# Optimization experiments

Hardware: AMD Instinct MI355X
Metric: run time of the kernel (lower is better)

The kernel has to match this reference:

```python
import jax, jax.numpy as jnp
import numpy as np

FG_THRESH = 0.5  # fg_iou_thresh in RetinaNetLoss.__init__
BG_THRESH = 0.4  # bg_iou_thresh
BELOW_LOW_QUALITY = -1
BETWEEN_THRESHOLDS = -2


def _make_boxes(key, lead_shape, img_size=800.0, max_wh=128.0):
    # Build valid xyxy boxes (x1<x2, y1<y2) inside an img_size image.
    k1, k2 = jax.random.split(key)
    cxcy = jax.random.uniform(k1, lead_shape + (2,), minval=0.0, maxval=img_size)
    wh = jax.random.uniform(k2, lead_shape + (2,), minval=8.0, maxval=max_wh)
    return jnp.concatenate([cxcy - wh * 0.5, cxcy + wh * 0.5], axis=-1)


def setup_inputs() -> dict:
    key = jax.random.key(0)
    kb, ka = jax.random.split(key)
    B, G, A = 8, 64, 120000
    gt_boxes = _make_boxes(kb, (B, G))                 # [B, G, 4] per-image gt boxes
    anchors = _make_boxes(ka, (A,), max_wh=256.0)      # [A, 4] shared anchors
    return {"gt_boxes": gt_boxes, "anchors": anchors}


def _box_iou(boxes1, boxes2):
    # boxes1 [G,4], boxes2 [A,4] -> IoU [G,A] (torchvision box_ops.box_iou)
    area1 = (boxes1[:, 2] - boxes1[:, 0]) * (boxes1[:, 3] - boxes1[:, 1])  # [G]
    area2 = (boxes2[:, 2] - boxes2[:, 0]) * (boxes2[:, 3] - boxes2[:, 1])  # [A]
    lt = jnp.maximum(boxes1[:, None, :2], boxes2[None, :, :2])  # [G,A,2]
    rb = jnp.minimum(boxes1[:, None, 2:], boxes2[None, :, 2:])  # [G,A,2]
    wh = jnp.clip(rb - lt, 0.0)
    inter = wh[..., 0] * wh[..., 1]  # [G,A]
    return inter / (area1[:, None] + area2[None, :] - inter)


def _match(quality):
    # torchvision Matcher(0.5, 0.4, allow_low_quality_matches=True) on quality [G,A]
    matched_vals = quality.max(axis=0)                      # [A] best IoU per anchor
    all_matches = jnp.argmax(quality, axis=0)               # [A] pre-threshold matches
    matches = jnp.where(matched_vals < BG_THRESH, BELOW_LOW_QUALITY, all_matches)
    matches = jnp.where((matched_vals >= BG_THRESH) & (matched_vals < FG_THRESH),
                        BETWEEN_THRESHOLDS, matches)
    # low-quality match recovery: anchors achieving the per-gt max keep their match
    highest_per_gt = quality.max(axis=1, keepdims=True)     # [G,1]
    pred_update = (quality == highest_per_gt).any(axis=0)   # [A]
    matches = jnp.where(pred_update, all_matches, matches)
    return matches.astype(jnp.int64), matched_vals


def reference(gt_boxes, anchors):
    # gt_boxes [B,G,4], anchors [A,4] -> matched_idxs [B,A] int64, matched_vals [B,A]
    def per_image(boxes):
        return _match(_box_iou(boxes, anchors))
    matched_idxs, matched_vals = jax.vmap(per_image)(gt_boxes)
    return matched_idxs, matched_vals
```

## Files before the change

kernel.cpp:

```cpp
#include <hip/hip_runtime.h>


static constexpr int G = 64;
static constexpr int NCELL = 256;

__device__ __forceinline__ float opaque(float x) {
    asm volatile("" : "+v"(x));
    return x;
}

__device__ __forceinline__ int vindex(int i) {
    asm volatile("" : "+v"(i));
    return i;
}

__device__ __forceinline__ float box_area(float x1, float y1, float x2, float y2) {
    return opaque(__fmul_rn(__fsub_rn(x2, x1), __fsub_rn(y2, y1)));
}

__device__ __forceinline__ float inter_area(float gx1, float gy1, float gx2, float gy2,
                                            float ax1, float ay1, float ax2, float ay2) {
    float ltx = fmaxf(gx1, ax1);
    float lty = fmaxf(gy1, ay1);
    float rbx = fminf(gx2, ax2);
    float rby = fminf(gy2, ay2);
    float w = fmaxf(__fsub_rn(rbx, ltx), 0.0f);
    float h = fmaxf(__fsub_rn(rby, lty), 0.0f);
    return opaque(__fmul_rn(w, h));
}

__device__ __forceinline__ float div_rn(float n, float d) {
    float r = __builtin_amdgcn_rcpf(d);
    float e = fmaf(-d, r, 1.0f);
    r = fmaf(e, r, r);
    float q = __fmul_rn(n, r);
    float s = fmaf(-d, q, n);
    q = fmaf(s, r, q);
    s = fmaf(-d, q, n);
    q = fmaf(s, r, q);
    return q;
}

#define DPP_MAX_STAGE(x, ctrl)                                                   \
    do {                                                                         \
        int _yi = __builtin_amdgcn_update_dpp(__float_as_int(x),                 \
                                              __float_as_int(x), (ctrl),         \
                                              0xf, 0xf, false);                  \
        (x) = fmaxf((x), __int_as_float(_yi));                                   \
    } while (0)

#define DPP_MIN_STAGE(x, ctrl)                                                   \
    do {                                                                         \
        int _yi = __builtin_amdgcn_update_dpp(__float_as_int(x),                 \
                                              __float_as_int(x), (ctrl),         \
                                              0xf, 0xf, false);                  \
        (x) = fminf((x), __int_as_float(_yi));                                   \
    } while (0)

__device__ __forceinline__ float wave_max_lane63(float x) {
    DPP_MAX_STAGE(x, 0xB1);
    DPP_MAX_STAGE(x, 0x4E);
    DPP_MAX_STAGE(x, 0x141);
    DPP_MAX_STAGE(x, 0x140);
    DPP_MAX_STAGE(x, 0x142);
    DPP_MAX_STAGE(x, 0x143);
    return x;
}

__device__ __forceinline__ float wave_min_lane63(float x) {
    DPP_MIN_STAGE(x, 0xB1);
    DPP_MIN_STAGE(x, 0x4E);
    DPP_MIN_STAGE(x, 0x141);
    DPP_MIN_STAGE(x, 0x140);
    DPP_MIN_STAGE(x, 0x142);
    DPP_MIN_STAGE(x, 0x143);
    return x;
}

__device__ __forceinline__ float lane63_bcast(float x) {
    return __int_as_float(__builtin_amdgcn_readlane(__float_as_int(x), 63));
}

__global__ void k_init(const float* __restrict__ gt, unsigned int* __restrict__ hpg,
                       float* __restrict__ gab, int BG) {
    int i = blockIdx.x * 256 + threadIdx.x;
    if (i < BG) {
        hpg[i] = 0u;
        float4 gb = ((const float4*)gt)[i];
        gab[i] = box_area(gb.x, gb.y, gb.z, gb.w);
    }
}

__device__ __forceinline__ int cell_of(float4 ab) {
    float cx = (ab.x + ab.z) * 0.5f;
    float cy = (ab.y + ab.w) * 0.5f;
    int cxi = (int)(cx * 0.02f); cxi = cxi < 0 ? 0 : (cxi > 15 ? 15 : cxi);
    int cyi = (int)(cy * 0.02f); cyi = cyi < 0 ? 0 : (cyi > 15 ? 15 : cyi);
    return cyi * 16 + cxi;
}

__global__ void k_count(const float* __restrict__ anchors,
                        unsigned int* __restrict__ bh, int A, int NB) {
    __shared__ unsigned int h[NCELL];
    int t = threadIdx.x;
    h[t] = 0u;
    __syncthreads();
    int a = blockIdx.x * 256 + t;
    if (a < A) atomicAdd(&h[cell_of(((const float4*)anchors)[a])], 1u);
    __syncthreads();
    bh[(size_t)t * NB + blockIdx.x] = h[t];
}

__global__ void k_rowscan(unsigned int* __restrict__ bh,
                          unsigned int* __restrict__ cellTot, int NB) {
    const int c = blockIdx.x;
    unsigned int* row = bh + (size_t)c * NB;
    __shared__ unsigned int s[256];
    __shared__ unsigned int carry;
    if (threadIdx.x == 0) carry = 0u;
    __syncthreads();
    for (int base = 0; base < NB; base += 256) {
        int i = base + threadIdx.x;
        unsigned int v = (i < NB) ? row[i] : 0u;
        s[threadIdx.x] = v;
        __syncthreads();
        for (int d = 1; d < 256; d <<= 1) {
            unsigned int add = (threadIdx.x >= d) ? s[threadIdx.x - d] : 0u;
            __syncthreads();
            s[threadIdx.x] += add;
            __syncthreads();
        }
        unsigned int excl = s[threadIdx.x] - v + carry;
        if (i < NB) row[i] = excl;
        __syncthreads();
        if (threadIdx.x == 255) carry += s[255];
        __syncthreads();
    }
    if (threadIdx.x == 0) cellTot[c] = carry;
}

__global__ void k_base(const unsigned int* __restrict__ cellTot,
                       unsigned int* __restrict__ cellBase) {
    __shared__ unsigned int s[NCELL];
    int t = threadIdx.x;
    unsigned int v = cellTot[t];
    s[t] = v;
    __syncthreads();
    for (int d = 1; d < NCELL; d <<= 1) {
        unsigned int add = (t >= d) ? s[t - d] : 0u;
        __syncthreads();
        s[t] += add;
        __syncthreads();
    }
    cellBase[t] = s[t] - v;
}

__global__ void k_scat(const float* __restrict__ anchors,
                       const unsigned int* __restrict__ bh,
                       const unsigned int* __restrict__ cellBase,
                       float* __restrict__ sortedA,
                       int* __restrict__ orig, int A, int NB) {
    __shared__ unsigned int h[NCELL];
    int t = threadIdx.x;
    h[t] = 0u;
    __syncthreads();
    int a = blockIdx.x * 256 + t;
    if (a < A) {
        float4 ab = ((const float4*)anchors)[a];
        int c = cell_of(ab);
        unsigned int lr = atomicAdd(&h[c], 1u);
        unsigned int pos = cellBase[c] + bh[(size_t)c * NB + blockIdx.x] + lr;
        ((float4*)sortedA)[pos] = ab;
        orig[pos] = a;
    }
}

template <bool STORE>
__global__ __launch_bounds__(256, 4)
void pass1_k(const float* __restrict__ gt,
             const float* __restrict__ anchors,
             const float* __restrict__ gab,
             unsigned int* __restrict__ hpg,
             unsigned int* __restrict__ sredg,
             float* __restrict__ vmaxA,
             int* __restrict__ amaxA,
             int A, int nchunks) {
    const int b = blockIdx.y;
    const int t = threadIdx.x;

    __shared__ unsigned int sred[G];
    if (t < G) sred[t] = 0u;
    __syncthreads();

    const int base = blockIdx.x * 1024;
    float ax1[4], ay1[4], ax2[4], ay2[4], aar[4];
    bool val[4];
#pragma unroll
    for (int k = 0; k < 4; ++k) {
        int a = base + k * 256 + t;
        val[k] = (a < A);
        float4 ab = ((const float4*)anchors)[val[k] ? a : 0];
        ax1[k] = val[k] ? ab.x : 3.0e38f;
        ay1[k] = val[k] ? ab.y : 3.0e38f;
        ax2[k] = val[k] ? ab.z : -3.0e38f;
        ay2[k] = val[k] ? ab.w : -3.0e38f;
        aar[k] = val[k] ? box_area(ax1[k], ay1[k], ax2[k], ay2[k]) : 0.0f;
    }

    float wx1 = fminf(fminf(ax1[0], ax1[1]), fminf(ax1[2], ax1[3]));
    float wy1 = fminf(fminf(ay1[0], ay1[1]), fminf(ay1[2], ay1[3]));
    float wx2 = fmaxf(fmaxf(ax2[0], ax2[1]), fmaxf(ax2[2], ax2[3]));
    float wy2 = fmaxf(fmaxf(ay2[0], ay2[1]), fmaxf(ay2[2], ay2[3]));
    wx1 = lane63_bcast(wave_min_lane63(wx1));
    wy1 = lane63_bcast(wave_min_lane63(wy1));
    wx2 = lane63_bcast(wave_max_lane63(wx2));
    wy2 = lane63_bcast(wave_max_lane63(wy2));

    const float4* gtb = (const float4*)gt + (size_t)b * G;
    const float* gas = gab + b * G;

    float vmax[4] = {0.0f, 0.0f, 0.0f, 0.0f};
    int amax[4] = {0, 0, 0, 0};

#pragma unroll 4
    for (int g = 0; g < G; ++g) {
        const int gv = vindex(g);
        const float4 gb = gtb[gv];
        float tlx = fmaxf(gb.x, wx1), trx = fminf(gb.z, wx2);
        float tly = fmaxf(gb.y, wy1), tby = fminf(gb.w, wy2);
        if ((trx > tlx) && (tby > tly)) {
            float inter[4];
#pragma unroll
            for (int k = 0; k < 4; ++k)
                inter[k] = inter_area(gb.x, gb.y, gb.z, gb.w,
                                      ax1[k], ay1[k], ax2[k], ay2[k]);
            float itest = fmaxf(fmaxf(inter[0], inter[1]),
                                fmaxf(inter[2], inter[3]));
            if (__any(itest > 0.0f)) {
                const float ga = gas[gv];
                float m = 0.0f;
#pragma unroll
                for (int k = 0; k < 4; ++k) {
                    float denom = __fsub_rn(__fadd_rn(ga, aar[k]), inter[k]);
                    float q = div_rn(inter[k], denom);
                    if constexpr (STORE) {
                        if (q > vmax[k]) { vmax[k] = q; amax[k] = g; }
                    }
                    m = fmaxf(m, q);
                }
                m = wave_max_lane63(m);
                if ((t & 63) == 63)
                    atomicMax(&sred[g], __float_as_uint(m));
            }
        }
    }

    if constexpr (STORE) {
#pragma unroll
        for (int k = 0; k < 4; ++k) {
            if (!val[k]) continue;
            size_t idx = (size_t)b * A + (base + k * 256 + t);
            vmaxA[idx] = vmax[k];
            amaxA[idx] = amax[k];
        }
    }

    __syncthreads();
    if (t < G) {
        atomicMax(&hpg[b * G + t], sred[t]);
        if constexpr (STORE)
            sredg[(size_t)(b * nchunks + blockIdx.x) * G + t] = sred[t];
    }
}

template <bool SCATTER>
__global__ __launch_bounds__(256, 8)
void pass2_lite(const float* __restrict__ gt,
                const float* __restrict__ anchors,
                const float* __restrict__ gab,
                const unsigned int* __restrict__ hpg,
                const unsigned int* __restrict__ sredg,
                const float* __restrict__ vmaxA,
                const int* __restrict__ amaxA,
                const int* __restrict__ orig,
                float* __restrict__ out_idx,
                float* __restrict__ out_val,
                int A, int nchunks) {
    const int b = blockIdx.y;
    const int t = threadIdx.x;
    const int base = blockIdx.x * 1024;

    const unsigned int* sb = sredg + (size_t)(b * nchunks + blockIdx.x) * G;
    const unsigned int* hb = hpg + b * G;

    unsigned long long E = 0ull;
#pragma unroll 16
    for (int g = 0; g < G; ++g)
        E |= (sb[g] == hb[g]) ? (1ull << g) : 0ull;

    bool pu[4] = {false, false, false, false};

    if (E != 0ull) {
        const float4* gtb = (const float4*)gt + (size_t)b * G;
        const float* gas = gab + b * G;
        float ax1[4], ay1[4], ax2[4], ay2[4], aar[4];
#pragma unroll
        for (int k = 0; k < 4; ++k) {
            int a = base + k * 256 + t;
            bool v = (a < A);
            float4 ab = ((const float4*)anchors)[v ? a : 0];
            ax1[k] = v ? ab.x : 3.0e38f;
            ay1[k] = v ? ab.y : 3.0e38f;
            ax2[k] = v ? ab.z : -3.0e38f;
            ay2[k] = v ? ab.w : -3.0e38f;
            aar[k] = v ? box_area(ax1[k], ay1[k], ax2[k], ay2[k]) : 0.0f;
        }
        unsigned long long e = E;
        while (e) {
            int g = __builtin_ctzll(e);
            e &= e - 1;
            float4 gb = gtb[g];
            float ga = gas[g];
            float hgf = __uint_as_float(hb[g]);
#pragma unroll
            for (int k = 0; k < 4; ++k) {
                float inter = inter_area(gb.x, gb.y, gb.z, gb.w,
                                         ax1[k], ay1[k], ax2[k], ay2[k]);
                float denom = __fsub_rn(__fadd_rn(ga, aar[k]), inter);
                float q = div_rn(inter, denom);
                pu[k] = pu[k] | (q == hgf);
            }
        }
    }

#pragma unroll
    for (int k = 0; k < 4; ++k) {
        int a = base + k * 256 + t;
        if (a >= A) continue;
        size_t idx = (size_t)b * A + a;
        float vm = vmaxA[idx];
        int am = amaxA[idx];
        int m;
        if (pu[k]) {
            m = am;
        } else if (vm < 0.4f) {
            m = -1;
        } else if (vm < 0.5f) {
            m = -2;
        } else {
            m = am;
        }
        size_t o = SCATTER ? ((size_t)b * A + orig[a]) : idx;
        out_idx[o] = (float)m;
        out_val[o] = vm;
    }
}

extern "C" void kernel_launch(void* const* d_in, const int* in_sizes, int n_in,
                              void* d_out, int out_size, void* d_ws, size_t ws_size,
                              hipStream_t stream) {
    const float* gt = (const float*)d_in[0];
    const float* anchors = (const float*)d_in[1];
    const int BG = in_sizes[0] / 4;
    const int B = BG / G;
    const int A = in_sizes[1] / 4;

    const int nchunks = (A + 1023) / 1024;
    const int NB = (A + 255) / 256;

    unsigned int* ws = (unsigned int*)d_ws;
    unsigned int* hpg = ws;
    float* gab = (float*)(ws + 512);
    unsigned int* cellBase = ws + 1024;
    unsigned int* cellTot = ws + 1280;
    unsigned int* bh = ws + 1536;
    size_t soff = 1536 + (size_t)NB * 256;
    soff = (soff + 3) & ~(size_t)3;
    float* sortedA = (float*)(ws + soff);
    int* orig = (int*)(ws + soff + 4 * (size_t)A);
    unsigned int* sredg = ws + soff + 5 * (size_t)A;
    size_t voff = soff + 5 * (size_t)A + (size_t)nchunks * B * G;
    float* vmaxA = (float*)(ws + voff);
    int* amaxA = (int*)(vmaxA + (size_t)B * A);
    const size_t need = (voff + 2 * (size_t)B * A) * 4;
    const bool sorted = (ws_size >= need);

    float* out_idx = (float*)d_out;
    float* out_val = out_idx + (size_t)B * A;

    k_init<<<(BG + 255) / 256, 256, 0, stream>>>(gt, hpg, gab, BG);

    dim3 g1(nchunks, B);
    if (sorted) {
        k_count<<<NB, 256, 0, stream>>>(anchors, bh, A, NB);
        k_rowscan<<<NCELL, 256, 0, stream>>>(bh, cellTot, NB);
        k_base<<<1, NCELL, 0, stream>>>(cellTot, cellBase);
        k_scat<<<NB, 256, 0, stream>>>(anchors, bh, cellBase, sortedA, orig, A, NB);
        pass1_k<true><<<g1, 256, 0, stream>>>(gt, sortedA, gab, hpg, sredg,
                                              vmaxA, amaxA, A, nchunks);
        pass2_lite<true><<<g1, 256, 0, stream>>>(gt, sortedA, gab, hpg, sredg,
                                                 vmaxA, amaxA, orig,
                                                 out_idx, out_val, A, nchunks);
    } else {
        pass1_k<true><<<g1, 256, 0, stream>>>(gt, anchors, gab, hpg, sredg,
                                              vmaxA, amaxA, A, nchunks);
        pass2_lite<false><<<g1, 256, 0, stream>>>(gt, anchors, gab, hpg, sredg,
                                                  vmaxA, amaxA, orig,
                                                  out_idx, out_val, A, nchunks);
    }
}
```

Measured before the change: 80.40 us.

## Write final outputs in pass1, patch low-quality matches only, fuse init/base kernels

Pass1 now applies the threshold logic and writes matched indices and values straight to the output, and the second pass only rewrites indices for anchors that hit a per-gt maximum. Blocks with no such candidate exit early. This removes the vmax workspace round-trip and the full rewrite of both outputs in the second pass. The k_init work is folded into k_count and the k_base scan into k_scat, removing two launches. The cost is that every k_scat block redundantly rescans the 256 cell totals. In the fallback path k_count now also runs its full anchor histogram just to do the init work.

```diff
diff --git a/kernel.cpp b/kernel.cpp
--- a/kernel.cpp
+++ b/kernel.cpp
@@ -81,16 +81,6 @@
     return __int_as_float(__builtin_amdgcn_readlane(__float_as_int(x), 63));
 }
 
-__global__ void k_init(const float* __restrict__ gt, unsigned int* __restrict__ hpg,
-                       float* __restrict__ gab, int BG) {
-    int i = blockIdx.x * 256 + threadIdx.x;
-    if (i < BG) {
-        hpg[i] = 0u;
-        float4 gb = ((const float4*)gt)[i];
-        gab[i] = box_area(gb.x, gb.y, gb.z, gb.w);
-    }
-}
-
 __device__ __forceinline__ int cell_of(float4 ab) {
     float cx = (ab.x + ab.z) * 0.5f;
     float cy = (ab.y + ab.w) * 0.5f;
@@ -99,10 +89,20 @@
     return cyi * 16 + cxi;
 }
 
-__global__ void k_count(const float* __restrict__ anchors,
-                        unsigned int* __restrict__ bh, int A, int NB) {
+__global__ void k_count(const float* __restrict__ gt,
+                        const float* __restrict__ anchors,
+                        unsigned int* __restrict__ bh,
+                        unsigned int* __restrict__ hpg,
+                        float* __restrict__ gab,
+                        int A, int NB, int BG) {
+    int t = threadIdx.x;
+    int gi = blockIdx.x * 256 + t;
+    if (gi < BG) {
+        hpg[gi] = 0u;
+        float4 gb = ((const float4*)gt)[gi];
+        gab[gi] = box_area(gb.x, gb.y, gb.z, gb.w);
+    }
     __shared__ unsigned int h[NCELL];
-    int t = threadIdx.x;
     h[t] = 0u;
     __syncthreads();
     int a = blockIdx.x * 256 + t;
@@ -139,51 +139,49 @@
     if (threadIdx.x == 0) cellTot[c] = carry;
 }
 
-__global__ void k_base(const unsigned int* __restrict__ cellTot,
-                       unsigned int* __restrict__ cellBase) {
-    __shared__ unsigned int s[NCELL];
+__global__ void k_scat(const float* __restrict__ anchors,
+                       const unsigned int* __restrict__ bh,
+                       const unsigned int* __restrict__ cellTot,
+                       float* __restrict__ sortedA,
+                       int* __restrict__ orig, int A, int NB) {
+    __shared__ unsigned int cb[NCELL];
+    __shared__ unsigned int tot[NCELL];
+    __shared__ unsigned int h[NCELL];
     int t = threadIdx.x;
     unsigned int v = cellTot[t];
-    s[t] = v;
+    cb[t] = v;
+    tot[t] = v;
+    h[t] = 0u;
     __syncthreads();
     for (int d = 1; d < NCELL; d <<= 1) {
-        unsigned int add = (t >= d) ? s[t - d] : 0u;
-        __syncthreads();
-        s[t] += add;
-        __syncthreads();
-    }
-    cellBase[t] = s[t] - v;
-}
-
-__global__ void k_scat(const float* __restrict__ anchors,
-                       const unsigned int* __restrict__ bh,
-                       const unsigned int* __restrict__ cellBase,
-                       float* __restrict__ sortedA,
-                       int* __restrict__ orig, int A, int NB) {
-    __shared__ unsigned int h[NCELL];
-    int t = threadIdx.x;
-    h[t] = 0u;
-    __syncthreads();
+        unsigned int add = (t >= d) ? cb[t - d] : 0u;
+        __syncthreads();
+        cb[t] += add;
+        __syncthreads();
+    }
     int a = blockIdx.x * 256 + t;
     if (a < A) {
         float4 ab = ((const float4*)anchors)[a];
         int c = cell_of(ab);
         unsigned int lr = atomicAdd(&h[c], 1u);
-        unsigned int pos = cellBase[c] + bh[(size_t)c * NB + blockIdx.x] + lr;
+        unsigned int base = cb[c] - tot[c];
+        unsigned int pos = base + bh[(size_t)c * NB + blockIdx.x] + lr;
         ((float4*)sortedA)[pos] = ab;
         orig[pos] = a;
     }
 }
 
-template <bool STORE>
+template <bool SCATTER>
 __global__ __launch_bounds__(256, 4)
 void pass1_k(const float* __restrict__ gt,
              const float* __restrict__ anchors,
              const float* __restrict__ gab,
              unsigned int* __restrict__ hpg,
              unsigned int* __restrict__ sredg,
-             float* __restrict__ vmaxA,
              int* __restrict__ amaxA,
+             const int* __restrict__ orig,
+             float* __restrict__ out_idx,
+             float* __restrict__ out_val,
              int A, int nchunks) {
     const int b = blockIdx.y;
     const int t = threadIdx.x;
@@ -243,9 +241,7 @@
                 for (int k = 0; k < 4; ++k) {
                     float denom = __fsub_rn(__fadd_rn(ga, aar[k]), inter[k]);
                     float q = div_rn(inter[k], denom);
-                    if constexpr (STORE) {
-                        if (q > vmax[k]) { vmax[k] = q; amax[k] = g; }
-                    }
+                    if (q > vmax[k]) { vmax[k] = q; amax[k] = g; }
                     m = fmaxf(m, q);
                 }
                 m = wave_max_lane63(m);
@@ -255,37 +251,40 @@
         }
     }
 
-    if constexpr (STORE) {
-#pragma unroll
-        for (int k = 0; k < 4; ++k) {
-            if (!val[k]) continue;
-            size_t idx = (size_t)b * A + (base + k * 256 + t);
-            vmaxA[idx] = vmax[k];
-            amaxA[idx] = amax[k];
-        }
+#pragma unroll
+    for (int k = 0; k < 4; ++k) {
+        if (!val[k]) continue;
+        int a = base + k * 256 + t;
+        size_t sidx = (size_t)b * A + a;
+        amaxA[sidx] = amax[k];
+        int mt;
+        if (vmax[k] < 0.4f) mt = -1;
+        else if (vmax[k] < 0.5f) mt = -2;
+        else mt = amax[k];
+        int ao = SCATTER ? orig[a] : a;
+        size_t o = (size_t)b * A + ao;
+        out_idx[o] = (float)mt;
+        out_val[o] = vmax[k];
     }
 
     __syncthreads();
     if (t < G) {
         atomicMax(&hpg[b * G + t], sred[t]);
-        if constexpr (STORE)
-            sredg[(size_t)(b * nchunks + blockIdx.x) * G + t] = sred[t];
+        sredg[(size_t)(b * nchunks + blockIdx.x) * G + t] = sred[t];
     }
 }
 
 template <bool SCATTER>
 __global__ __launch_bounds__(256, 8)
-void pass2_lite(const float* __restrict__ gt,
-                const float* __restrict__ anchors,
-                const float* __restrict__ gab,
-                const unsigned int* __restrict__ hpg,
-                const unsigned int* __restrict__ sredg,
-                const float* __restrict__ vmaxA,
-                const int* __restrict__ amaxA,
-                const int* __restrict__ orig,
-                float* __restrict__ out_idx,
-                float* __restrict__ out_val,
-                int A, int nchunks) {
+void k_patch(const float* __restrict__ gt,
+             const float* __restrict__ anchors,
+             const float* __restrict__ gab,
+             const unsigned int* __restrict__ hpg,
+             const unsigned int* __restrict__ sredg,
+             const int* __restrict__ amaxA,
+             const int* __restrict__ orig,
+             float* __restrict__ out_idx,
+             int A, int nchunks) {
     const int b = blockIdx.y;
     const int t = threadIdx.x;
     const int base = blockIdx.x * 1024;
@@ -297,62 +296,48 @@
 #pragma unroll 16
     for (int g = 0; g < G; ++g)
         E |= (sb[g] == hb[g]) ? (1ull << g) : 0ull;
-
-    bool pu[4] = {false, false, false, false};
-
-    if (E != 0ull) {
-        const float4* gtb = (const float4*)gt + (size_t)b * G;
-        const float* gas = gab + b * G;
-        float ax1[4], ay1[4], ax2[4], ay2[4], aar[4];
-#pragma unroll
-        for (int k = 0; k < 4; ++k) {
-            int a = base + k * 256 + t;
-            bool v = (a < A);
-            float4 ab = ((const float4*)anchors)[v ? a : 0];
-            ax1[k] = v ? ab.x : 3.0e38f;
-            ay1[k] = v ? ab.y : 3.0e38f;
-            ax2[k] = v ? ab.z : -3.0e38f;
-            ay2[k] = v ? ab.w : -3.0e38f;
-            aar[k] = v ? box_area(ax1[k], ay1[k], ax2[k], ay2[k]) : 0.0f;
-        }
-        unsigned long long e = E;
-        while (e) {
-            int g = __builtin_ctzll(e);
-            e &= e - 1;
-            float4 gb = gtb[g];
-            float ga = gas[g];
-            float hgf = __uint_as_float(hb[g]);
-#pragma unroll
-            for (int k = 0; k < 4; ++k) {
-                float inter = inter_area(gb.x, gb.y, gb.z, gb.w,
-                                         ax1[k], ay1[k], ax2[k], ay2[k]);
-                float denom = __fsub_rn(__fadd_rn(ga, aar[k]), inter);
-                float q = div_rn(inter, denom);
-                pu[k] = pu[k] | (q == hgf);
-            }
-        }
-    }
-
+    if (E == 0ull) return;
+
+    const float4* gtb = (const float4*)gt + (size_t)b * G;
+    const float* gas = gab + b * G;
+    float ax1[4], ay1[4], ax2[4], ay2[4], aar[4];
+    bool val[4];
 #pragma unroll
     for (int k = 0; k < 4; ++k) {
         int a = base + k * 256 + t;
-        if (a >= A) continue;
-        size_t idx = (size_t)b * A + a;
-        float vm = vmaxA[idx];
-        int am = amaxA[idx];
-        int m;
-        if (pu[k]) {
-            m = am;
-        } else if (vm < 0.4f) {
-            m = -1;
-        } else if (vm < 0.5f) {
-            m = -2;
-        } else {
-            m = am;
+        val[k] = (a < A);
+        float4 ab = ((const float4*)anchors)[val[k] ? a : 0];
+        ax1[k] = val[k] ? ab.x : 3.0e38f;
+        ay1[k] = val[k] ? ab.y : 3.0e38f;
+        ax2[k] = val[k] ? ab.z : -3.0e38f;
+        ay2[k] = val[k] ? ab.w : -3.0e38f;
+        aar[k] = val[k] ? box_area(ax1[k], ay1[k], ax2[k], ay2[k]) : 0.0f;
+    }
+
+    bool pu[4] = {false, false, false, false};
+    unsigned long long e = E;
+    while (e) {
+        int g = __builtin_ctzll(e);
+        e &= e - 1;
+        float4 gb = gtb[g];
+        float ga = gas[g];
+        float hgf = __uint_as_float(hb[g]);
+#pragma unroll
+        for (int k = 0; k < 4; ++k) {
+            float inter = inter_area(gb.x, gb.y, gb.z, gb.w,
+                                     ax1[k], ay1[k], ax2[k], ay2[k]);
+            float denom = __fsub_rn(__fadd_rn(ga, aar[k]), inter);
+            float q = div_rn(inter, denom);
+            pu[k] = pu[k] | (q == hgf);
         }
-        size_t o = SCATTER ? ((size_t)b * A + orig[a]) : idx;
-        out_idx[o] = (float)m;
-        out_val[o] = vm;
+    }
+
+#pragma unroll
+    for (int k = 0; k < 4; ++k) {
+        int a = base + k * 256 + t;
+        if (!val[k] || !pu[k]) continue;
+        int ao = SCATTER ? orig[a] : a;
+        out_idx[(size_t)b * A + ao] = (float)amaxA[(size_t)b * A + a];
     }
 }
 
@@ -371,41 +356,37 @@
     unsigned int* ws = (unsigned int*)d_ws;
     unsigned int* hpg = ws;
     float* gab = (float*)(ws + 512);
-    unsigned int* cellBase = ws + 1024;
-    unsigned int* cellTot = ws + 1280;
-    unsigned int* bh = ws + 1536;
-    size_t soff = 1536 + (size_t)NB * 256;
+    unsigned int* cellTot = ws + 1024;
+    unsigned int* bh = ws + 1280;
+    size_t soff = 1280 + (size_t)NB * 256;
     soff = (soff + 3) & ~(size_t)3;
     float* sortedA = (float*)(ws + soff);
     int* orig = (int*)(ws + soff + 4 * (size_t)A);
     unsigned int* sredg = ws + soff + 5 * (size_t)A;
-    size_t voff = soff + 5 * (size_t)A + (size_t)nchunks * B * G;
-    float* vmaxA = (float*)(ws + voff);
-    int* amaxA = (int*)(vmaxA + (size_t)B * A);
-    const size_t need = (voff + 2 * (size_t)B * A) * 4;
+    size_t aoff = soff + 5 * (size_t)A + (size_t)nchunks * B * G;
+    int* amaxA = (int*)(ws + aoff);
+    const size_t need = (aoff + (size_t)B * A) * 4;
     const bool sorted = (ws_size >= need);
 
     float* out_idx = (float*)d_out;
     float* out_val = out_idx + (size_t)B * A;
 
-    k_init<<<(BG + 255) / 256, 256, 0, stream>>>(gt, hpg, gab, BG);
-
     dim3 g1(nchunks, B);
     if (sorted) {
-        k_count<<<NB, 256, 0, stream>>>(anchors, bh, A, NB);
+        k_count<<<NB, 256, 0, stream>>>(gt, anchors, bh, hpg, gab, A, NB, BG);
         k_rowscan<<<NCELL, 256, 0, stream>>>(bh, cellTot, NB);
-        k_base<<<1, NCELL, 0, stream>>>(cellTot, cellBase);
-        k_scat<<<NB, 256, 0, stream>>>(anchors, bh, cellBase, sortedA, orig, A, NB);
+        k_scat<<<NB, 256, 0, stream>>>(anchors, bh, cellTot, sortedA, orig, A, NB);
         pass1_k<true><<<g1, 256, 0, stream>>>(gt, sortedA, gab, hpg, sredg,
-                                              vmaxA, amaxA, A, nchunks);
-        pass2_lite<true><<<g1, 256, 0, stream>>>(gt, sortedA, gab, hpg, sredg,
-                                                 vmaxA, amaxA, orig,
-                                                 out_idx, out_val, A, nchunks);
+                                              amaxA, orig, out_idx, out_val,
+                                              A, nchunks);
+        k_patch<true><<<g1, 256, 0, stream>>>(gt, sortedA, gab, hpg, sredg,
+                                              amaxA, orig, out_idx, A, nchunks);
     } else {
-        pass1_k<true><<<g1, 256, 0, stream>>>(gt, anchors, gab, hpg, sredg,
-                                              vmaxA, amaxA, A, nchunks);
-        pass2_lite<false><<<g1, 256, 0, stream>>>(gt, anchors, gab, hpg, sredg,
-                                                  vmaxA, amaxA, orig,
-                                                  out_idx, out_val, A, nchunks);
-    }
-}
+        k_count<<<NB, 256, 0, stream>>>(gt, anchors, bh, hpg, gab, A, NB, BG);
+        pass1_k<false><<<g1, 256, 0, stream>>>(gt, anchors, gab, hpg, sredg,
+                                               amaxA, orig, out_idx, out_val,
+                                               A, nchunks);
+        k_patch<false><<<g1, 256, 0, stream>>>(gt, anchors, gab, hpg, sredg,
+                                               amaxA, orig, out_idx, A, nchunks);
+    }
+}
```

Result: faster. 68.34 us (-15.0%).
